# Kernel optimization log

Hardware: AMD Instinct MI355X
Metric: run time of the kernel (lower is better)

## Reference

```python
import jax, jax.numpy as jnp
import numpy as np

TREE_DEPTH = 6
TEMPERATURE = 1.0


def setup_inputs() -> dict:
    key = jax.random.key(0)
    k1, k2, k3, k4, k5 = jax.random.split(key, 5)
    B, D = 8192, 512
    T = 64                      # n_trees
    N = 2 ** TREE_DEPTH - 1    # internal nodes = 63
    L = 2 ** TREE_DEPTH        # leaves = 64
    C = 100                    # classes
    return {
        "x": jax.random.normal(k1, (B, D), dtype=jnp.float32),
        "split_weights": jax.random.normal(k2, (T, N, D), dtype=jnp.float32),
        "split_bias": jax.random.normal(k3, (T, N), dtype=jnp.float32),
        "leaf_logits": jax.random.normal(k4, (T, L, C), dtype=jnp.float32),
        "tree_weights": jax.random.uniform(k5, (T,), dtype=jnp.float32),
    }


def reference(x, split_weights, split_bias, leaf_logits, tree_weights):
    # All node decisions for all trees in one batched GEMM: [B, T, N]
    dec = jax.nn.sigmoid(
        (jnp.einsum("bd,tnd->btn", x, split_weights) + split_bias) / TEMPERATURE
    )
    B = x.shape[0]
    T = split_weights.shape[0]
    L = leaf_logits.shape[1]  # 2 ** TREE_DEPTH
    leaf_ids = jnp.arange(L)
    # Cumulative product of routing probs along each leaf's root-to-leaf path.
    leaf_probs = jnp.ones((B, T, L), dtype=x.dtype)
    for d in range(TREE_DEPTH):
        # ancestor node (level order) of each leaf at this depth
        node_idx = (2 ** d - 1) + (leaf_ids >> (TREE_DEPTH - d))
        # 1 -> right child (prob = dec), 0 -> left child (prob = 1 - dec)
        bit = (leaf_ids >> (TREE_DEPTH - d - 1)) & 1
        dd = dec[:, :, node_idx]  # [B, T, L]
        leaf_probs = leaf_probs * jnp.where(bit.astype(bool), dd, 1.0 - dd)
    tree_out = jax.nn.softmax(leaf_logits, axis=-1)  # [T, L, C]
    # weighted sum over trees of (leaf_probs @ leaf class dists)
    return jnp.einsum("btl,tlc,t->bc", leaf_probs, tree_out, tree_weights)
```

## Files before the change

### kernel.cpp

```cpp
#include <hip/hip_runtime.h>

#define TREES 64
#define NN 63
#define LL 64
#define CC 100
#define CPAD 112
#define DD 512
#define BB 8192

typedef __attribute__((ext_vector_type(8))) _Float16 f16x8;
typedef __attribute__((ext_vector_type(4))) _Float16 f16x4;
typedef __attribute__((ext_vector_type(4))) float floatx4;

#define XH_WS   0
#define SWH_WS  8388608
#define W2T_WS  12582912
#define LP_WS   13500416

__device__ __forceinline__ void gl_lds16(const _Float16* g, char* lds) {
    __builtin_amdgcn_global_load_lds(
        (const __attribute__((address_space(1))) unsigned int*)g,
        (__attribute__((address_space(3))) unsigned int*)lds, 16, 0, 0);
}

__device__ __forceinline__ f16x8 cvt8(const float* s) {
    float4 a = *(const float4*)s, b = *(const float4*)(s + 4);
    f16x8 h;
    h[0]=(_Float16)a.x; h[1]=(_Float16)a.y; h[2]=(_Float16)a.z; h[3]=(_Float16)a.w;
    h[4]=(_Float16)b.x; h[5]=(_Float16)b.y; h[6]=(_Float16)b.z; h[7]=(_Float16)b.w;
    return h;
}

__global__ __launch_bounds__(256) void prep_kernel(
    const float* __restrict__ x, const float* __restrict__ sw,
    const float* __restrict__ leaf_logits, const float* __restrict__ tree_w,
    _Float16* __restrict__ xh, _Float16* __restrict__ swh,
    _Float16* __restrict__ w2T)
{
    if (blockIdx.x < 3072) {
        int i = blockIdx.x * 256 + threadIdx.x;
        if (i < 524288) {
            int tile = i >> 10, cidx = i & 1023;
            int row = cidx >> 3, c = cidx & 7;
            int rb = tile >> 3, kt = tile & 7;
            int gk = kt * 64 + ((c ^ (row & 7)) << 3);
            *(f16x8*)(xh + (size_t)i * 8) = cvt8(x + (size_t)(rb * 128 + row) * DD + gk);
        } else {
            int j = i - 524288;
            if (j < 262144) {
                int tile = j >> 10, cidx = j & 1023;
                int col = cidx >> 3, c = cidx & 7;
                int cb = tile >> 3, kt = tile & 7;
                int tt = col >> 6, node = col & 63;
                f16x8 h = (f16x8)(_Float16)0.f;
                if (node < NN) {
                    int gk = kt * 64 + ((c ^ (col & 7)) << 3);
                    h = cvt8(sw + (size_t)((cb * 2 + tt) * NN + node) * DD + gk);
                }
                *(f16x8*)(swh + (size_t)j * 8) = h;
            }
        }
    } else {
        int row  = (blockIdx.x - 3072) * 4 + (threadIdx.x >> 6);
        int lane = threadIdx.x & 63;
        int t = row >> 6, l = row & 63;
        const float* src = leaf_logits + (size_t)row * CC;
        float v0 = (lane < CC)      ? src[lane]      : -1e30f;
        float v1 = (lane + 64 < CC) ? src[lane + 64] : -1e30f;
        float m = fmaxf(v0, v1);
#pragma unroll
        for (int off = 32; off > 0; off >>= 1)
            m = fmaxf(m, __shfl_down(m, off, 64));
        m = __shfl(m, 0, 64);
        float e0 = (lane < CC)      ? __expf(v0 - m) : 0.f;
        float e1 = (lane + 64 < CC) ? __expf(v1 - m) : 0.f;
        float s = e0 + e1;
#pragma unroll
        for (int off = 32; off > 0; off >>= 1)
            s += __shfl_down(s, off, 64);
        s = __shfl(s, 0, 64);
        float scale = tree_w[t] / s;
        _Float16* base = w2T + (size_t)t * CPAD * LL;
#define LSWZ(c) ((((l >> 3) ^ ((c) & 7)) << 3) | (l & 7))
        if (lane < CC)      base[(size_t)lane * LL + LSWZ(lane)]               = (_Float16)(e0 * scale);
        if (lane + 64 < CC) base[(size_t)(lane + 64) * LL + LSWZ(lane + 64)]   = (_Float16)(e1 * scale);
        if (lane < CPAD - CC) base[(size_t)(CC + lane) * LL + LSWZ(CC + lane)] = (_Float16)0.f;
#undef LSWZ
    }
}

#define A_SMEM 33280
__global__ __launch_bounds__(256, 4) void gemm1_kernel(
    const _Float16* __restrict__ xh,
    const _Float16* __restrict__ swh,
    const float* __restrict__ sb,
    _Float16* __restrict__ lp_ws)
{
    __shared__ __align__(16) char smem[A_SMEM];
    _Float16* xs  = (_Float16*)smem;
    _Float16* wl  = (_Float16*)(smem + 16384);
    _Float16* dec = (_Float16*)smem;
    _Float16* lpl = (_Float16*)smem;

    const int tid  = threadIdx.x;
    const int lane = tid & 63;
    const int wid  = tid >> 6;
    const int wy   = wid >> 1;
    const int wx   = wid & 1;
    const int quad = lane >> 4;
    const int l15  = lane & 15;
    const int rb   = blockIdx.x;
    const int cb   = blockIdx.y;

    float bias_v[4];
    {
        int mytree = cb * 2 + wx;
#pragma unroll
        for (int ni = 0; ni < 4; ++ni) {
            int nd = 16 * ni + l15;
            bias_v[ni] = (nd < NN) ? sb[mytree * NN + nd] : 0.f;
        }
    }

    floatx4 acc[4][4];
#pragma unroll
    for (int i = 0; i < 4; ++i)
#pragma unroll
        for (int j = 0; j < 4; ++j) acc[i][j] = (floatx4)0.f;

    const _Float16* xtile = xh + (size_t)rb * 8 * 8192;
    const _Float16* wtile = swh + (size_t)cb * 8 * 8192;

    for (int kt = 0; kt < 8; ++kt) {
        __syncthreads();
#pragma unroll
        for (int j = 0; j < 4; ++j) {
            gl_lds16(xtile + kt * 8192 + j * 2048 + wid * 512 + lane * 8,
                     smem + j * 4096 + wid * 1024);
            gl_lds16(wtile + kt * 8192 + j * 2048 + wid * 512 + lane * 8,
                     smem + 16384 + j * 4096 + wid * 1024);
        }
        __syncthreads();
#pragma unroll
        for (int ks = 0; ks < 2; ++ks) {
            f16x8 af[4], bf[4];
#pragma unroll
            for (int mi = 0; mi < 4; ++mi) {
                int r = 64 * wy + 16 * mi + l15;
                af[mi] = *(const f16x8*)&xs[r * 64 + ((((ks << 2) | quad) ^ (r & 7)) << 3)];
            }
#pragma unroll
            for (int ni = 0; ni < 4; ++ni) {
                int r = 64 * wx + 16 * ni + l15;
                bf[ni] = *(const f16x8*)&wl[r * 64 + ((((ks << 2) | quad) ^ (r & 7)) << 3)];
            }
#pragma unroll
            for (int mi = 0; mi < 4; ++mi)
#pragma unroll
                for (int ni = 0; ni < 4; ++ni)
                    acc[mi][ni] = __builtin_amdgcn_mfma_f32_16x16x32_f16(
                        af[mi], bf[ni], acc[mi][ni], 0, 0, 0);
        }
    }
    __syncthreads();

#pragma unroll
    for (int mi = 0; mi < 4; ++mi) {
        int r0 = 64 * wy + 16 * mi + 4 * quad;
#pragma unroll
        for (int ni = 0; ni < 4; ++ni) {
            int col = 64 * wx + 16 * ni + l15;
            f16x4 v;
#pragma unroll
            for (int r = 0; r < 4; ++r)
                v[r] = (_Float16)(acc[mi][ni][r] + bias_v[ni]);
            *(f16x4*)&dec[col * 130 + r0] = v;
        }
    }
    __syncthreads();

    const int tt   = tid >> 7;
    const int lrow = tid & 127;
    const int tb   = tt * 64;
    f16x8 lpreg[8];
    {
#define SIG(n) (1.f / (1.f + __expf(-(float)dec[(tb + (n)) * 130 + lrow])))
        float d0 = SIG(0);
#pragma unroll
        for (int h = 0; h < 2; ++h) {
            float p1 = h ? d0 : 1.f - d0;
            float d1 = SIG(1 + h);
#pragma unroll
            for (int b8 = 0; b8 < 4; ++b8) {
                int i4 = b8 >> 1, i3 = b8 & 1;
                float p2 = p1 * (i4 ? d1 : 1.f - d1);
                float d2 = SIG(3 + 2 * h + i4);
                float p3 = p2 * (i3 ? d2 : 1.f - d2);
                float d3 = SIG(7 + 4 * h + b8);
                f16x8 blk;
#pragma unroll
                for (int i2 = 0; i2 < 2; ++i2) {
                    float p4 = p3 * (i2 ? d3 : 1.f - d3);
                    float d4 = SIG(15 + 8 * h + 2 * b8 + i2);
#pragma unroll
                    for (int i1 = 0; i1 < 2; ++i1) {
                        float p5 = p4 * (i1 ? d4 : 1.f - d4);
                        float d5 = SIG(31 + 16 * h + 4 * b8 + 2 * i2 + i1);
                        blk[i2 * 4 + i1 * 2 + 0] = (_Float16)(p5 * (1.f - d5));
                        blk[i2 * 4 + i1 * 2 + 1] = (_Float16)(p5 * d5);
                    }
                }
                lpreg[h * 4 + b8] = blk;
            }
        }
#undef SIG
    }
    __syncthreads();

#pragma unroll
    for (int q = 0; q < 8; ++q)
        *(f16x8*)&lpl[tt * 8192 + lrow * 64 + ((q ^ (lrow & 7)) << 3)] = lpreg[q];
    __syncthreads();

    const int rloc0 = blockIdx.x * 128;
#pragma unroll
    for (int k = 0; k < 8; ++k) {
        int idx = k * 256 + tid;
        int t2 = idx >> 10, rem = idx & 1023;
        int row = rem >> 3, cq = rem & 7;
        f16x8 v = *(const f16x8*)&lpl[t2 * 8192 + row * 64 + cq * 8];
        *(f16x8*)(lp_ws + ((size_t)(cb * 2 + t2) * BB + rloc0 + row) * 64 + cq * 8) = v;
    }
}

#define RSTR 113
#define RREG (32 * RSTR)
__global__ __launch_bounds__(512, 2) void gemm2_kernel(
    const _Float16* __restrict__ lp_ws,
    const _Float16* __restrict__ w2T,
    float* __restrict__ out)
{
    __shared__ float red[4 * RREG];

    const int tid  = threadIdx.x;
    const int lane = tid & 63;
    const int wv   = tid >> 6;
    const int quad = lane >> 4;
    const int l15  = lane & 15;
    const int r0   = blockIdx.x * 32;
    const int t0   = wv * 8;

    floatx4 oacc[2][7];
#pragma unroll
    for (int mi = 0; mi < 2; ++mi)
#pragma unroll
        for (int ni = 0; ni < 7; ++ni) oacc[mi][ni] = (floatx4)0.f;

    const int sw0 = ((0 | quad) ^ (l15 & 7)) << 3;
    const int sw1 = ((4 | quad) ^ (l15 & 7)) << 3;
    const _Float16* aBase = lp_ws + ((size_t)t0 * BB + r0 + l15) * 64;
    const _Float16* bBase = w2T + (size_t)t0 * CPAD * LL + (size_t)l15 * 64;

    f16x8 ab[2][2], bb[2][7];
#define LOADS(s, buf)                                                          \
    {                                                                          \
        int t8 = (s) >> 1;                                                     \
        int sw = ((s) & 1) ? sw1 : sw0;                                        \
        const _Float16* ap = aBase + (size_t)t8 * (BB * 64);                   \
        const _Float16* bp = bBase + (size_t)t8 * (CPAD * LL);                 \
        ab[buf][0] = *(const f16x8*)(ap + sw);                                 \
        ab[buf][1] = *(const f16x8*)(ap + 16 * 64 + sw);                       \
        _Pragma("unroll")                                                      \
        for (int ni = 0; ni < 7; ++ni)                                         \
            bb[buf][ni] = *(const f16x8*)(bp + ni * 16 * 64 + sw);             \
    }
#define MFMAS(buf)                                                             \
    {                                                                          \
        _Pragma("unroll")                                                      \
        for (int mi = 0; mi < 2; ++mi)                                         \
            _Pragma("unroll")                                                  \
            for (int ni = 0; ni < 7; ++ni)                                     \
                oacc[mi][ni] = __builtin_amdgcn_mfma_f32_16x16x32_f16(         \
                    ab[buf][mi], bb[buf][ni], oacc[mi][ni], 0, 0, 0);          \
    }
    LOADS(0, 0)
#pragma unroll
    for (int s = 0; s < 15; ++s) {
        LOADS(s + 1, (s + 1) & 1)
        MFMAS(s & 1)
    }
    MFMAS(1)
#undef LOADS
#undef MFMAS

    if (wv >= 4) {
        float* rg = &red[(wv - 4) * RREG];
#pragma unroll
        for (int mi = 0; mi < 2; ++mi)
#pragma unroll
            for (int ni = 0; ni < 7; ++ni)
#pragma unroll
                for (int r = 0; r < 4; ++r)
                    rg[(16 * mi + 4 * quad + r) * RSTR + 16 * ni + l15] = oacc[mi][ni][r];
    }
    __syncthreads();
    if (wv < 4) {
        float* rg = &red[wv * RREG];
#pragma unroll
        for (int mi = 0; mi < 2; ++mi)
#pragma unroll
            for (int ni = 0; ni < 7; ++ni)
#pragma unroll
                for (int r = 0; r < 4; ++r)
                    rg[(16 * mi + 4 * quad + r) * RSTR + 16 * ni + l15] += oacc[mi][ni][r];
    }
    __syncthreads();
    {
        int row = tid >> 4, c16 = tid & 15;
#pragma unroll
        for (int k = 0; k < 7; ++k) {
            int col = k * 16 + c16;
            float s = 0.f;
#pragma unroll
            for (int g = 0; g < 4; ++g)
                s += red[g * RREG + row * RSTR + col];
            if (col < CC)
                out[(size_t)(r0 + row) * CC + col] = s;
        }
    }
}

extern "C" void kernel_launch(void* const* d_in, const int* in_sizes, int n_in,
                              void* d_out, int out_size, void* d_ws, size_t ws_size,
                              hipStream_t stream) {
    const float* x  = (const float*)d_in[0];
    const float* sw = (const float*)d_in[1];
    const float* sb = (const float*)d_in[2];
    const float* ll = (const float*)d_in[3];
    const float* tw = (const float*)d_in[4];
    float* out = (float*)d_out;
    _Float16* xh  = (_Float16*)((char*)d_ws + XH_WS);
    _Float16* swh = (_Float16*)((char*)d_ws + SWH_WS);
    _Float16* w2T = (_Float16*)((char*)d_ws + W2T_WS);
    _Float16* lp  = (_Float16*)((char*)d_ws + LP_WS);

    prep_kernel<<<dim3(4096), 256, 0, stream>>>(x, sw, ll, tw, xh, swh, w2T);
    gemm1_kernel<<<dim3(64, 32), 256, 0, stream>>>(xh, swh, sb, lp);
    gemm2_kernel<<<dim3(256), 512, 0, stream>>>(lp, w2T, out);
}
```

Before: 161.6 us.

## Process two row tiles per gemm1 block to reuse split-weight tiles

Each gemm1 block now computes two 128-row batch tiles against the same weight tile. The weight slab is loaded once into LDS and reused for both, which halves the grid and the weight traffic per output. The change doubles the accumulator registers, raises LDS to 48KB and drops the occupancy hint. Sigmoid now uses a hardware reciprocal instead of a division.

New measurement: 188.2 us. 1.16x slower.

```diff
diff --git a/kernel.cpp b/kernel.cpp
--- a/kernel.cpp
+++ b/kernel.cpp
@@ -29,6 +29,10 @@
     h[0]=(_Float16)a.x; h[1]=(_Float16)a.y; h[2]=(_Float16)a.z; h[3]=(_Float16)a.w;
     h[4]=(_Float16)b.x; h[5]=(_Float16)b.y; h[6]=(_Float16)b.z; h[7]=(_Float16)b.w;
     return h;
+}
+
+__device__ __forceinline__ float fsig(float x) {
+    return __builtin_amdgcn_rcpf(1.f + __expf(-x));
 }
 
 __global__ __launch_bounds__(256) void prep_kernel(
@@ -89,16 +93,17 @@
     }
 }
 
-#define A_SMEM 33280
-__global__ __launch_bounds__(256, 4) void gemm1_kernel(
+#define A_SMEM 49152
+__global__ __launch_bounds__(256) void gemm1_kernel(
     const _Float16* __restrict__ xh,
     const _Float16* __restrict__ swh,
     const float* __restrict__ sb,
     _Float16* __restrict__ lp_ws)
 {
     __shared__ __align__(16) char smem[A_SMEM];
-    _Float16* xs  = (_Float16*)smem;
-    _Float16* wl  = (_Float16*)(smem + 16384);
+    _Float16* xsA = (_Float16*)smem;
+    _Float16* xsB = (_Float16*)(smem + 16384);
+    _Float16* wl  = (_Float16*)(smem + 32768);
     _Float16* dec = (_Float16*)smem;
     _Float16* lpl = (_Float16*)smem;
 
@@ -109,7 +114,6 @@
     const int wx   = wid & 1;
     const int quad = lane >> 4;
     const int l15  = lane & 15;
-    const int rb   = blockIdx.x;
     const int cb   = blockIdx.y;
 
     float bias_v[4];
@@ -122,32 +126,37 @@
         }
     }
 
-    floatx4 acc[4][4];
-#pragma unroll
-    for (int i = 0; i < 4; ++i)
-#pragma unroll
-        for (int j = 0; j < 4; ++j) acc[i][j] = (floatx4)0.f;
-
-    const _Float16* xtile = xh + (size_t)rb * 8 * 8192;
-    const _Float16* wtile = swh + (size_t)cb * 8 * 8192;
+    floatx4 acc[2][4][4];
+#pragma unroll
+    for (int rb = 0; rb < 2; ++rb)
+#pragma unroll
+        for (int i = 0; i < 4; ++i)
+#pragma unroll
+            for (int j = 0; j < 4; ++j) acc[rb][i][j] = (floatx4)0.f;
+
+    const _Float16* xtileA = xh + (size_t)(blockIdx.x * 2)     * 8 * 8192;
+    const _Float16* xtileB = xh + (size_t)(blockIdx.x * 2 + 1) * 8 * 8192;
+    const _Float16* wtile  = swh + (size_t)cb * 8 * 8192;
 
     for (int kt = 0; kt < 8; ++kt) {
         __syncthreads();
 #pragma unroll
         for (int j = 0; j < 4; ++j) {
-            gl_lds16(xtile + kt * 8192 + j * 2048 + wid * 512 + lane * 8,
-                     smem + j * 4096 + wid * 1024);
-            gl_lds16(wtile + kt * 8192 + j * 2048 + wid * 512 + lane * 8,
-                     smem + 16384 + j * 4096 + wid * 1024);
+            int off = (j * 256 + tid) * 8;
+            gl_lds16(xtileA + kt * 8192 + off, smem +         off * 2);
+            gl_lds16(xtileB + kt * 8192 + off, smem + 16384 + off * 2);
+            gl_lds16(wtile  + kt * 8192 + off, smem + 32768 + off * 2);
         }
         __syncthreads();
 #pragma unroll
         for (int ks = 0; ks < 2; ++ks) {
-            f16x8 af[4], bf[4];
+            f16x8 afA[4], afB[4], bf[4];
 #pragma unroll
             for (int mi = 0; mi < 4; ++mi) {
                 int r = 64 * wy + 16 * mi + l15;
-                af[mi] = *(const f16x8*)&xs[r * 64 + ((((ks << 2) | quad) ^ (r & 7)) << 3)];
+                int so = r * 64 + ((((ks << 2) | quad) ^ (r & 7)) << 3);
+                afA[mi] = *(const f16x8*)&xsA[so];
+                afB[mi] = *(const f16x8*)&xsB[so];
             }
 #pragma unroll
             for (int ni = 0; ni < 4; ++ni) {
@@ -157,79 +166,85 @@
 #pragma unroll
             for (int mi = 0; mi < 4; ++mi)
 #pragma unroll
-                for (int ni = 0; ni < 4; ++ni)
-                    acc[mi][ni] = __builtin_amdgcn_mfma_f32_16x16x32_f16(
-                        af[mi], bf[ni], acc[mi][ni], 0, 0, 0);
-        }
-    }
-    __syncthreads();
-
-#pragma unroll
-    for (int mi = 0; mi < 4; ++mi) {
-        int r0 = 64 * wy + 16 * mi + 4 * quad;
-#pragma unroll
-        for (int ni = 0; ni < 4; ++ni) {
-            int col = 64 * wx + 16 * ni + l15;
-            f16x4 v;
-#pragma unroll
-            for (int r = 0; r < 4; ++r)
-                v[r] = (_Float16)(acc[mi][ni][r] + bias_v[ni]);
-            *(f16x4*)&dec[col * 130 + r0] = v;
-        }
-    }
-    __syncthreads();
-
-    const int tt   = tid >> 7;
-    const int lrow = tid & 127;
-    const int tb   = tt * 64;
-    f16x8 lpreg[8];
-    {
-#define SIG(n) (1.f / (1.f + __expf(-(float)dec[(tb + (n)) * 130 + lrow])))
-        float d0 = SIG(0);
-#pragma unroll
-        for (int h = 0; h < 2; ++h) {
-            float p1 = h ? d0 : 1.f - d0;
-            float d1 = SIG(1 + h);
-#pragma unroll
-            for (int b8 = 0; b8 < 4; ++b8) {
-                int i4 = b8 >> 1, i3 = b8 & 1;
-                float p2 = p1 * (i4 ? d1 : 1.f - d1);
-                float d2 = SIG(3 + 2 * h + i4);
-                float p3 = p2 * (i3 ? d2 : 1.f - d2);
-                float d3 = SIG(7 + 4 * h + b8);
-                f16x8 blk;
-#pragma unroll
-                for (int i2 = 0; i2 < 2; ++i2) {
-                    float p4 = p3 * (i2 ? d3 : 1.f - d3);
-                    float d4 = SIG(15 + 8 * h + 2 * b8 + i2);
-#pragma unroll
-                    for (int i1 = 0; i1 < 2; ++i1) {
-                        float p5 = p4 * (i1 ? d4 : 1.f - d4);
-                        float d5 = SIG(31 + 16 * h + 4 * b8 + 2 * i2 + i1);
-                        blk[i2 * 4 + i1 * 2 + 0] = (_Float16)(p5 * (1.f - d5));
-                        blk[i2 * 4 + i1 * 2 + 1] = (_Float16)(p5 * d5);
+                for (int ni = 0; ni < 4; ++ni) {
+                    acc[0][mi][ni] = __builtin_amdgcn_mfma_f32_16x16x32_f16(
+                        afA[mi], bf[ni], acc[0][mi][ni], 0, 0, 0);
+                    acc[1][mi][ni] = __builtin_amdgcn_mfma_f32_16x16x32_f16(
+                        afB[mi], bf[ni], acc[1][mi][ni], 0, 0, 0);
+                }
+        }
+    }
+
+    for (int rb = 0; rb < 2; ++rb) {
+        __syncthreads();
+
+#pragma unroll
+        for (int mi = 0; mi < 4; ++mi) {
+            int r0 = 64 * wy + 16 * mi + 4 * quad;
+#pragma unroll
+            for (int ni = 0; ni < 4; ++ni) {
+                int col = 64 * wx + 16 * ni + l15;
+                f16x4 v;
+#pragma unroll
+                for (int r = 0; r < 4; ++r)
+                    v[r] = (_Float16)(acc[rb][mi][ni][r] + bias_v[ni]);
+                *(f16x4*)&dec[col * 130 + r0] = v;
+            }
+        }
+        __syncthreads();
+
+        const int tt   = tid >> 7;
+        const int lrow = tid & 127;
+        const int tb   = tt * 64;
+        f16x8 lpreg[8];
+        {
+#define SIG(n) fsig((float)dec[(tb + (n)) * 130 + lrow])
+            float d0 = SIG(0);
+#pragma unroll
+            for (int h = 0; h < 2; ++h) {
+                float p1 = h ? d0 : 1.f - d0;
+                float d1 = SIG(1 + h);
+#pragma unroll
+                for (int b8 = 0; b8 < 4; ++b8) {
+                    int i4 = b8 >> 1, i3 = b8 & 1;
+                    float p2 = p1 * (i4 ? d1 : 1.f - d1);
+                    float d2 = SIG(3 + 2 * h + i4);
+                    float p3 = p2 * (i3 ? d2 : 1.f - d2);
+                    float d3 = SIG(7 + 4 * h + b8);
+                    f16x8 blk;
+#pragma unroll
+                    for (int i2 = 0; i2 < 2; ++i2) {
+                        float p4 = p3 * (i2 ? d3 : 1.f - d3);
+                        float d4 = SIG(15 + 8 * h + 2 * b8 + i2);
+#pragma unroll
+                        for (int i1 = 0; i1 < 2; ++i1) {
+                            float p5 = p4 * (i1 ? d4 : 1.f - d4);
+                            float d5 = SIG(31 + 16 * h + 4 * b8 + 2 * i2 + i1);
+                            blk[i2 * 4 + i1 * 2 + 0] = (_Float16)(p5 * (1.f - d5));
+                            blk[i2 * 4 + i1 * 2 + 1] = (_Float16)(p5 * d5);
+                        }
                     }
+                    lpreg[h * 4 + b8] = blk;
                 }
-                lpreg[h * 4 + b8] = blk;
-            }
-        }
+            }
 #undef SIG
-    }
-    __syncthreads();
-
-#pragma unroll
-    for (int q = 0; q < 8; ++q)
-        *(f16x8*)&lpl[tt * 8192 + lrow * 64 + ((q ^ (lrow & 7)) << 3)] = lpreg[q];
-    __syncthreads();
-
-    const int rloc0 = blockIdx.x * 128;
-#pragma unroll
-    for (int k = 0; k < 8; ++k) {
-        int idx = k * 256 + tid;
-        int t2 = idx >> 10, rem = idx & 1023;
-        int row = rem >> 3, cq = rem & 7;
-        f16x8 v = *(const f16x8*)&lpl[t2 * 8192 + row * 64 + cq * 8];
-        *(f16x8*)(lp_ws + ((size_t)(cb * 2 + t2) * BB + rloc0 + row) * 64 + cq * 8) = v;
+        }
+        __syncthreads();
+
+#pragma unroll
+        for (int q = 0; q < 8; ++q)
+            *(f16x8*)&lpl[tt * 8192 + lrow * 64 + ((q ^ (lrow & 7)) << 3)] = lpreg[q];
+        __syncthreads();
+
+        const int rloc0 = (blockIdx.x * 2 + rb) * 128;
+#pragma unroll
+        for (int k = 0; k < 8; ++k) {
+            int idx = k * 256 + tid;
+            int t2 = idx >> 10, rem = idx & 1023;
+            int row = rem >> 3, cq = rem & 7;
+            f16x8 v = *(const f16x8*)&lpl[t2 * 8192 + row * 64 + cq * 8];
+            *(f16x8*)(lp_ws + ((size_t)(cb * 2 + t2) * BB + rloc0 + row) * 64 + cq * 8) = v;
+        }
     }
 }
 
@@ -345,6 +360,6 @@
     _Float16* lp  = (_Float16*)((char*)d_ws + LP_WS);
 
     prep_kernel<<<dim3(4096), 256, 0, stream>>>(x, sw, ll, tw, xh, swh, w2T);
-    gemm1_kernel<<<dim3(64, 32), 256, 0, stream>>>(xh, swh, sb, lp);
+    gemm1_kernel<<<dim3(32, 32), 256, 0, stream>>>(xh, swh, sb, lp);
     gemm2_kernel<<<dim3(256), 512, 0, stream>>>(lp, w2T, out);
 }
```
